# Performance work log

Hardware: AMD Instinct MI355X
Metric: run time of the kernel (lower is better)

The kernel has to match this reference:

```python
import jax, jax.numpy as jnp
import numpy as np

B, S, NX, H = 8, 1024, 1024, 16
HD = NX // H  # head dim = 64
MASKED_BIAS = -10000.0


def setup_inputs() -> dict:
    key = jax.random.key(0)
    ks = jax.random.split(key, 6)
    return {
        "x": jax.random.normal(ks[0], (B, S, NX), dtype=jnp.float32),
        "query": jax.random.normal(ks[1], (B, S, NX), dtype=jnp.float32),
        "c_attn_w": jax.random.normal(ks[2], (NX, 3 * NX), dtype=jnp.float32) * 0.02,
        "c_attn_b": jnp.zeros((3 * NX,), dtype=jnp.float32),
        "c_proj_w": jax.random.normal(ks[3], (NX, NX), dtype=jnp.float32) * 0.02,
        "c_proj_b": jnp.zeros((NX,), dtype=jnp.float32),
    }


def _split_heads(t):
    # [B, S, NX] -> [B, H, S, HD]
    b, s, _ = t.shape
    return t.reshape(b, s, H, HD).transpose(0, 2, 1, 3)


def reference(x, query, c_attn_w, c_attn_b, c_proj_w, c_proj_b):
    # Conv1D: y = x @ W + b
    kv = x @ c_attn_w + c_attn_b          # [B,S,3NX]; use key/value slices
    qy = query @ c_attn_w + c_attn_b      # [B,S,3NX]; use query slice
    q = _split_heads(qy[..., :NX])                     # [B,H,S,HD]
    k = _split_heads(kv[..., NX:2 * NX])               # [B,H,S,HD]
    v = _split_heads(kv[..., 2 * NX:])                 # [B,H,S,HD]

    w = jnp.einsum("bhqd,bhkd->bhqk", q, k) / jnp.sqrt(jnp.float32(HD))
    causal = jnp.tril(jnp.ones((S, S), dtype=bool))[None, None]
    w = jnp.where(causal, w, jnp.float32(MASKED_BIAS))
    w = jax.nn.softmax(w, axis=-1)
    a = jnp.einsum("bhqk,bhkd->bhqd", w, v)            # [B,H,S,HD]
    a = a.transpose(0, 2, 1, 3).reshape(B, S, NX)      # merge heads
    return a @ c_proj_w + c_proj_b
```

## Files before the change

kernel.cpp:

```cpp
#include <hip/hip_runtime.h>
#include <cstdint>
#include <cstddef>

#define Bb   8
#define Ss   1024
#define NXx  1024
#define Hh   16
#define HDd  64
#define Mm   (Bb*Ss)

typedef __bf16 bf16x8 __attribute__((ext_vector_type(8)));
typedef float  f32x4  __attribute__((ext_vector_type(4)));

__device__ __forceinline__ unsigned short f2bf(float f) {
    union { float f; unsigned int u; } v; v.f = f;
    return (unsigned short)((v.u + 0x8000u) >> 16);
}
__device__ __forceinline__ unsigned int f2bf_hi(float f) {
    union { float f; unsigned int u; } v; v.f = f;
    return (v.u + 0x8000u) & 0xffff0000u;
}

__device__ __forceinline__ void load_lds16(const unsigned short* g, unsigned short* lds_base) {
    __builtin_amdgcn_global_load_lds(
        (const __attribute__((address_space(1))) void*)g,
        (__attribute__((address_space(3))) void*)lds_base, 16, 0, 0);
}

__global__ __launch_bounds__(256) void prep(
    const float* __restrict__ x, const float* __restrict__ query,
    const float* __restrict__ caw, const float* __restrict__ cpw,
    unsigned short* __restrict__ xb, unsigned short* __restrict__ qb,
    unsigned short* __restrict__ Wt, unsigned short* __restrict__ Pt)
{
    __shared__ float tile[32][33];
    const int bid = blockIdx.x;
    const int tid = threadIdx.x;

    if (bid < 16384) {
        const float* in = (bid < 8192) ? x : query;
        unsigned short* out = (bid < 8192) ? xb : qb;
        const int i = ((bid & 8191) * 256 + tid) * 4;
        const float4 v = *(const float4*)(in + i);
        unsigned long long p = (unsigned long long)f2bf(v.x)
            | ((unsigned long long)f2bf(v.y) << 16)
            | ((unsigned long long)f2bf(v.z) << 32)
            | ((unsigned long long)f2bf(v.w) << 48);
        *(unsigned long long*)(out + i) = p;
        return;
    }

    const float* in;
    unsigned short* out;
    int C, t;
    if (bid < 16384 + 3072) { in = caw; out = Wt; C = 3072; t = bid - 16384; }
    else                    { in = cpw; out = Pt; C = 1024; t = bid - 19456; }
    const int ntx = C >> 5;
    const int c0 = (t % ntx) * 32, r0 = (t / ntx) * 32;
    const int tx = tid & 31, ty = tid >> 5;
    for (int i = ty; i < 32; i += 8)
        tile[i][tx] = in[(size_t)(r0 + i) * C + c0 + tx];
    __syncthreads();
    for (int i = ty; i < 32; i += 8)
        out[(size_t)(c0 + i) * 1024 + r0 + tx] = f2bf(tile[tx][i]);
}

__global__ __launch_bounds__(256) void gemm128(
    const unsigned short* __restrict__ Ax,
    const unsigned short* __restrict__ Aq,
    const unsigned short* __restrict__ Bt,
    const float* __restrict__ bias,
    int K, int mode,
    unsigned short* __restrict__ out_q,
    unsigned short* __restrict__ out_k,
    unsigned short* __restrict__ out_v,
    float* __restrict__ out_f)
{
    __shared__ unsigned short smem[16384];
    unsigned short (*As)[64] = (unsigned short (*)[64])(smem);
    unsigned short (*Bs)[64] = (unsigned short (*)[64])(smem + 8192);

    const int tid  = threadIdx.x;
    const int w    = tid >> 6;
    const int lane = tid & 63;

    const int nx   = (mode == 0) ? 24 : 8;
    const int nxh  = nx >> 1;
    const int n    = blockIdx.x;
    const int xcd  = n & 7;
    const int sgrp = n >> 3;
    const int m0   = ((xcd >> 1) * 16 + sgrp / nxh) * 128;
    const int n0   = ((xcd & 1) * nxh + sgrp % nxh) * 128;
    const int region = n0 >> 10;
    const unsigned short* A = (mode == 0 && region == 0) ? Aq : Ax;

    const int wm   = (w >> 1) * 64;
    const int wn   = (w & 1) * 64;
    const int lrow = lane & 15;
    const int quad = lane >> 4;

    f32x4 acc[4][4] = {};

    const int rr   = lane >> 3;
    const int scol = (((lane & 7) ^ (lane >> 3)) << 3);
    const unsigned short* Ag = A  + (size_t)(m0 + w * 32 + rr) * K + scol;
    const unsigned short* Bg = Bt + (size_t)(n0 + w * 32 + rr) * K + scol;
    unsigned short* ldsA = smem + (w * 32) * 64;
    unsigned short* ldsB = smem + 8192 + (w * 32) * 64;

    const int swz = lrow & 7;

    for (int k0 = 0; k0 < K; k0 += 64) {
        __syncthreads();
#pragma unroll
        for (int c = 0; c < 4; ++c) {
            load_lds16(Ag + (size_t)(c * 8) * K + k0, ldsA + c * 512);
            load_lds16(Bg + (size_t)(c * 8) * K + k0, ldsB + c * 512);
        }
        __syncthreads();
#pragma unroll
        for (int kk = 0; kk < 2; ++kk) {
            bf16x8 af[4], bfr[4];
            const int pc = (((kk * 4 + quad) ^ swz) << 3);
#pragma unroll
            for (int i = 0; i < 4; ++i) {
                af[i]  = *(const bf16x8*)&As[wm + i * 16 + lrow][pc];
                bfr[i] = *(const bf16x8*)&Bs[wn + i * 16 + lrow][pc];
            }
#pragma unroll
            for (int i = 0; i < 4; ++i)
#pragma unroll
                for (int j = 0; j < 4; ++j)
                    acc[i][j] = __builtin_amdgcn_mfma_f32_16x16x32_bf16(af[i], bfr[j], acc[i][j], 0, 0, 0);
        }
    }

    __syncthreads();

    if (mode == 1) {
#pragma unroll
        for (int i = 0; i < 4; ++i)
#pragma unroll
            for (int j = 0; j < 4; ++j) {
                const int ncol = n0 + wn + j * 16 + lrow;
                const float bv = bias[ncol];
#pragma unroll
                for (int r = 0; r < 4; ++r) {
                    const int mrow = m0 + wm + i * 16 + quad * 4 + r;
                    out_f[(size_t)mrow * NXx + ncol] = acc[i][j][r] + bv;
                }
            }
        return;
    }

    unsigned short* ep = smem + w * 2048;

    if (region != 2) {
        unsigned short* outp = (region == 0) ? out_q : out_k;
#pragma unroll
        for (int j = 0; j < 4; ++j) {
            const float bv = bias[n0 + wn + j * 16 + lrow];
#pragma unroll
            for (int i = 0; i < 4; ++i)
#pragma unroll
                for (int r = 0; r < 4; ++r)
                    ep[(i * 16 + quad * 4 + r) * 24 + lrow] = f2bf(acc[i][j][r] + bv);
#pragma unroll
            for (int t = 0; t < 2; ++t) {
                const int c    = t * 64 + lane;
                const int row  = c >> 1, ch = (c & 1) * 8;
                const int mrow = m0 + wm + row;
                const int cc   = (n0 + wn + j * 16 + ch) & (NXx - 1);
                const int hh   = cc >> 6, dd = cc & 63;
                const int bh   = (mrow >> 10) * Hh + hh;
                const int ss   = mrow & (Ss - 1);
                *(uint4*)&outp[((size_t)bh * Ss + ss) * HDd + dd] =
                    *(const uint4*)&ep[row * 24 + ch];
            }
        }
    } else {
#pragma unroll
        for (int j = 0; j < 4; ++j) {
            const float bv = bias[n0 + wn + j * 16 + lrow];
#pragma unroll
            for (int i = 0; i < 4; ++i)
#pragma unroll
                for (int r = 0; r < 4; ++r)
                    ep[lrow * 72 + i * 16 + quad * 4 + r] = f2bf(acc[i][j][r] + bv);
#pragma unroll
            for (int t = 0; t < 2; ++t) {
                const int c    = t * 64 + lane;
                const int col  = c >> 3, rc = (c & 7) * 8;
                const int cc   = (n0 + wn + j * 16 + col) & (NXx - 1);
                const int hh   = cc >> 6, dd = cc & 63;
                const int mrow = m0 + wm + rc;
                const int bh   = (mrow >> 10) * Hh + hh;
                const int ss   = mrow & (Ss - 1);
                *(uint4*)&out_v[((size_t)bh * HDd + dd) * Ss + ss] =
                    *(const uint4*)&ep[col * 72 + rc];
            }
        }
    }
}

__global__ __launch_bounds__(512, 2) void gemm256(
    const unsigned short* __restrict__ Ax,
    const unsigned short* __restrict__ Aq,
    const unsigned short* __restrict__ Bt,
    const float* __restrict__ bias,
    unsigned short* __restrict__ out_q,
    unsigned short* __restrict__ out_k,
    unsigned short* __restrict__ out_v)
{
    __shared__ unsigned short lds[65536];

    const int tid  = threadIdx.x;
    const int w    = tid >> 6;
    const int lane = tid & 63;
    const int wm   = w >> 2;
    const int wn   = w & 3;
    const int lrow = lane & 15;
    const int quad = lane >> 4;
    const int swz  = lrow & 7;
    const int ca   = (quad ^ swz) << 3;
    const int cb   = ((4 + quad) ^ swz) << 3;

    const int n    = blockIdx.x;
    const int xcd  = n & 7;
    const int sg   = n >> 3;
    const int mi   = (xcd >> 1) * 8 + (sg & 7);
    const int ni   = (xcd & 1) * 6 + (sg >> 3);
    const int m0   = mi << 8;
    const int n0   = ni << 8;
    const int region = n0 >> 10;
    const unsigned short* A = (region == 0) ? Aq : Ax;

    const int srow = lane >> 3;
    const int chnk = (((lane & 7) ^ srow) << 3);
    const unsigned short* pA0 = A  + (size_t)(m0 +       w * 8 + srow) * 1024 + chnk;
    const unsigned short* pA1 = A  + (size_t)(m0 +  64 + w * 8 + srow) * 1024 + chnk;
    const unsigned short* pA2 = A  + (size_t)(m0 + 128 + w * 8 + srow) * 1024 + chnk;
    const unsigned short* pA3 = A  + (size_t)(m0 + 192 + w * 8 + srow) * 1024 + chnk;
    const unsigned short* pB0 = Bt + (size_t)(n0 +       w * 8 + srow) * 1024 + chnk;
    const unsigned short* pB1 = Bt + (size_t)(n0 +  64 + w * 8 + srow) * 1024 + chnk;
    const unsigned short* pB2 = Bt + (size_t)(n0 + 128 + w * 8 + srow) * 1024 + chnk;
    const unsigned short* pB3 = Bt + (size_t)(n0 + 192 + w * 8 + srow) * 1024 + chnk;
    const int wl = w * 512;

    f32x4 acc[8][4] = {};

    load_lds16(pA0, lds + 0 * 4096 + wl);
    load_lds16(pA2, lds + 2 * 4096 + wl);
    load_lds16(pB0, lds + 16384 + 0 * 4096 + wl);
    load_lds16(pB1, lds + 16384 + 1 * 4096 + wl);
    load_lds16(pB2, lds + 16384 + 2 * 4096 + wl);
    load_lds16(pB3, lds + 16384 + 3 * 4096 + wl);
    load_lds16(pA1, lds + 1 * 4096 + wl);
    load_lds16(pA3, lds + 3 * 4096 + wl);
    pA0 += 64; pA1 += 64; pA2 += 64; pA3 += 64;
    pB0 += 64; pB1 += 64; pB2 += 64; pB3 += 64;

    asm volatile("s_waitcnt vmcnt(2)" ::: "memory");
    __builtin_amdgcn_s_barrier();
    asm volatile("" ::: "memory");

#pragma unroll 1
    for (int t = 0; t < 16; ++t) {
        const int as = (t & 1) << 15;
        const int us = ((t & 1) ^ 1) << 15;
        const bool st = (t < 15);
        const int rbA = as + (wm * 128 + lrow) * 64;
        const int rbB = as + 16384 + (wn * 64 + lrow) * 64;

        bf16x8 a0f[4], a1f[4], b0q[4], b1q[4];

#pragma unroll
        for (int i = 0; i < 4; ++i) a0f[i] = *(const bf16x8*)&lds[rbA + i * 1024 + ca];
#pragma unroll
        for (int j = 0; j < 4; ++j) b0q[j] = *(const bf16x8*)&lds[rbB + j * 1024 + ca];
        if (st) {
            load_lds16(pA0, lds + us + 0 * 4096 + wl);
            load_lds16(pA2, lds + us + 2 * 4096 + wl);
            load_lds16(pB0, lds + us + 16384 + 0 * 4096 + wl);
        }
        __builtin_amdgcn_s_barrier();
        asm volatile("s_waitcnt lgkmcnt(0)" ::: "memory");
        __builtin_amdgcn_s_setprio(1);
#pragma unroll
        for (int i = 0; i < 4; ++i)
#pragma unroll
            for (int j = 0; j < 4; ++j)
                acc[i][j] = __builtin_amdgcn_mfma_f32_16x16x32_bf16(a0f[i], b0q[j], acc[i][j], 0, 0, 0);
        __builtin_amdgcn_s_setprio(0);
        asm volatile("" ::: "memory");
        __builtin_amdgcn_s_barrier();
        asm volatile("" ::: "memory");

#pragma unroll
        for (int i = 0; i < 4; ++i) a1f[i] = *(const bf16x8*)&lds[rbA + i * 1024 + cb];
#pragma unroll
        for (int j = 0; j < 4; ++j) b1q[j] = *(const bf16x8*)&lds[rbB + j * 1024 + cb];
        if (st) {
            load_lds16(pB1, lds + us + 16384 + 1 * 4096 + wl);
            load_lds16(pB2, lds + us + 16384 + 2 * 4096 + wl);
            load_lds16(pB3, lds + us + 16384 + 3 * 4096 + wl);
        }
        __builtin_amdgcn_s_barrier();
        asm volatile("s_waitcnt lgkmcnt(0)" ::: "memory");
        __builtin_amdgcn_s_setprio(1);
#pragma unroll
        for (int i = 0; i < 4; ++i)
#pragma unroll
            for (int j = 0; j < 4; ++j)
                acc[i][j] = __builtin_amdgcn_mfma_f32_16x16x32_bf16(a1f[i], b1q[j], acc[i][j], 0, 0, 0);
        __builtin_amdgcn_s_setprio(0);
        if (st) asm volatile("s_waitcnt vmcnt(6)" ::: "memory");
        else    asm volatile("s_waitcnt vmcnt(0)" ::: "memory");
        asm volatile("" ::: "memory");
        __builtin_amdgcn_s_barrier();
        asm volatile("" ::: "memory");

#pragma unroll
        for (int i = 0; i < 4; ++i) a0f[i] = *(const bf16x8*)&lds[rbA + 4096 + i * 1024 + ca];
        __builtin_amdgcn_s_barrier();
        asm volatile("s_waitcnt lgkmcnt(0)" ::: "memory");
        __builtin_amdgcn_s_setprio(1);
#pragma unroll
        for (int i = 0; i < 4; ++i)
#pragma unroll
            for (int j = 0; j < 4; ++j)
                acc[4 + i][j] = __builtin_amdgcn_mfma_f32_16x16x32_bf16(a0f[i], b0q[j], acc[4 + i][j], 0, 0, 0);
        __builtin_amdgcn_s_setprio(0);
        asm volatile("" ::: "memory");
        __builtin_amdgcn_s_barrier();
        asm volatile("" ::: "memory");

#pragma unroll
        for (int i = 0; i < 4; ++i) a1f[i] = *(const bf16x8*)&lds[rbA + 4096 + i * 1024 + cb];
        if (st) {
            load_lds16(pA1, lds + us + 1 * 4096 + wl);
            load_lds16(pA3, lds + us + 3 * 4096 + wl);
            pA0 += 64; pA1 += 64; pA2 += 64; pA3 += 64;
            pB0 += 64; pB1 += 64; pB2 += 64; pB3 += 64;
        }
        __builtin_amdgcn_s_barrier();
        asm volatile("s_waitcnt lgkmcnt(0)" ::: "memory");
        __builtin_amdgcn_s_setprio(1);
#pragma unroll
        for (int i = 0; i < 4; ++i)
#pragma unroll
            for (int j = 0; j < 4; ++j)
                acc[4 + i][j] = __builtin_amdgcn_mfma_f32_16x16x32_bf16(a1f[i], b1q[j], acc[4 + i][j], 0, 0, 0);
        __builtin_amdgcn_s_setprio(0);
        if (st) asm volatile("s_waitcnt vmcnt(2)" ::: "memory");
        asm volatile("" ::: "memory");
        __builtin_amdgcn_s_barrier();
        asm volatile("" ::: "memory");
    }

    __syncthreads();

    unsigned short* ep = lds + w * 8192;

    if (region != 2) {
        unsigned short* outp = (region == 0) ? out_q : out_k;
#pragma unroll
        for (int j = 0; j < 4; ++j) {
            const float bv = bias[n0 + wn * 64 + j * 16 + lrow];
#pragma unroll
            for (int i = 0; i < 8; ++i)
#pragma unroll
                for (int r = 0; r < 4; ++r)
                    ep[(i * 16 + quad * 4 + r) * 24 + lrow] = f2bf(acc[i][j][r] + bv);
#pragma unroll
            for (int tt = 0; tt < 4; ++tt) {
                const int c    = tt * 64 + lane;
                const int row  = c >> 1, ch = (c & 1) * 8;
                const int mrow = m0 + wm * 128 + row;
                const int cc   = (n0 + wn * 64 + j * 16 + ch) & (NXx - 1);
                const int hh   = cc >> 6, dd = cc & 63;
                const int bh   = (mrow >> 10) * Hh + hh;
                const int ss   = mrow & (Ss - 1);
                *(uint4*)&outp[((size_t)bh * Ss + ss) * HDd + dd] =
                    *(const uint4*)&ep[row * 24 + ch];
            }
        }
    } else {
#pragma unroll
        for (int j = 0; j < 4; ++j) {
            const float bv = bias[n0 + wn * 64 + j * 16 + lrow];
#pragma unroll
            for (int i = 0; i < 8; ++i)
#pragma unroll
                for (int r = 0; r < 4; ++r)
                    ep[lrow * 136 + i * 16 + quad * 4 + r] = f2bf(acc[i][j][r] + bv);
#pragma unroll
            for (int tt = 0; tt < 4; ++tt) {
                const int c    = tt * 64 + lane;
                const int col  = c >> 4, rc = (c & 15) * 8;
                const int cc   = (n0 + wn * 64 + j * 16 + col) & (NXx - 1);
                const int hh   = cc >> 6, dd = cc & 63;
                const int mrow = m0 + wm * 128 + rc;
                const int bh   = (mrow >> 10) * Hh + hh;
                const int ss   = mrow & (Ss - 1);
                *(uint4*)&out_v[((size_t)bh * HDd + dd) * Ss + ss] =
                    *(const uint4*)&ep[col * 136 + rc];
            }
        }
    }
}

__global__ __launch_bounds__(256) void flash_attn(
    const unsigned short* __restrict__ Qh,
    const unsigned short* __restrict__ Kh,
    const unsigned short* __restrict__ Vt,
    unsigned short* __restrict__ about)
{
    __shared__ unsigned short Ks[64][64];
    __shared__ unsigned short Vs[64][64];
    __shared__ unsigned short Pl[4][32][72];

    const int tid  = threadIdx.x;
    const int w    = tid >> 6;
    const int lane = tid & 63;
    const int bh   = blockIdx.x & 127;
    const int pr   = blockIdx.x >> 7;
    const int b    = bh >> 4, h = bh & 15;
    const int lrow = lane & 15;
    const int quad = lane >> 4;

    const unsigned short* Qb = Qh + (size_t)bh * Ss * HDd;
    const unsigned short* Kb = Kh + (size_t)bh * Ss * HDd;
    const unsigned short* Vb = Vt + (size_t)bh * HDd * Ss;

    const int sr = lane >> 3;
    const int lc = (((lane & 7) ^ (lane >> 3)) << 3);
    unsigned short* ldsK0 = &Ks[w * 16][0];
    unsigned short* ldsK1 = &Ks[w * 16 + 8][0];
    unsigned short* ldsV0 = &Vs[w * 16][0];
    unsigned short* ldsV1 = &Vs[w * 16 + 8][0];

    const int swz = lrow & 7;
    const int ca = ((quad ^ swz) << 3);
    const int cb = (((4 + quad) ^ swz) << 3);

    for (int half = 0; half < 2; ++half) {
        const int qt = half ? (7 - pr) : pr;
        const int qw = qt * 128 + w * 32;

        bf16x8 aq[2][2];
#pragma unroll
        for (int g = 0; g < 2; ++g)
#pragma unroll
            for (int c = 0; c < 2; ++c)
                aq[g][c] = *(const bf16x8*)(Qb + (size_t)(qw + g * 16 + lrow) * HDd + c * 32 + quad * 8);

        f32x4 O[2][4] = {};
        float lsum[2] = { 0.f, 0.f };

        const int nkt = 2 * qt + 2;
        for (int kt = 0; kt < nkt; ++kt) {
            const int k0 = kt * 64;

            __syncthreads();
            load_lds16(Kb + (size_t)(k0 + w * 16 + sr) * HDd + lc,     ldsK0);
            load_lds16(Kb + (size_t)(k0 + w * 16 + sr + 8) * HDd + lc, ldsK1);
            load_lds16(Vb + (size_t)(w * 16 + sr) * Ss + k0 + lc,      ldsV0);
            load_lds16(Vb + (size_t)(w * 16 + sr + 8) * Ss + k0 + lc,  ldsV1);
            __syncthreads();

            if (k0 > qw + 31) continue;

            f32x4 st[2][4] = {};
#pragma unroll
            for (int j = 0; j < 4; ++j) {
                const bf16x8 kf0 = *(const bf16x8*)&Ks[j * 16 + lrow][ca];
                const bf16x8 kf1 = *(const bf16x8*)&Ks[j * 16 + lrow][cb];
                st[0][j] = __builtin_amdgcn_mfma_f32_16x16x32_bf16(kf0, aq[0][0], st[0][j], 0, 0, 0);
                st[0][j] = __builtin_amdgcn_mfma_f32_16x16x32_bf16(kf1, aq[0][1], st[0][j], 0, 0, 0);
                st[1][j] = __builtin_amdgcn_mfma_f32_16x16x32_bf16(kf0, aq[1][0], st[1][j], 0, 0, 0);
                st[1][j] = __builtin_amdgcn_mfma_f32_16x16x32_bf16(kf1, aq[1][1], st[1][j], 0, 0, 0);
            }

            const bool needMask = (k0 + 63 > qw);
#pragma unroll
            for (int g = 0; g < 2; ++g) {
                const int qg = qw + g * 16 + lrow;
#pragma unroll
                for (int j = 0; j < 4; ++j) {
                    const int kbase = k0 + j * 16 + quad * 4;
                    float e0 = __expf(st[g][j][0] * 0.125f);
                    float e1 = __expf(st[g][j][1] * 0.125f);
                    float e2 = __expf(st[g][j][2] * 0.125f);
                    float e3 = __expf(st[g][j][3] * 0.125f);
                    if (needMask) {
                        if (kbase     > qg) e0 = 0.f;
                        if (kbase + 1 > qg) e1 = 0.f;
                        if (kbase + 2 > qg) e2 = 0.f;
                        if (kbase + 3 > qg) e3 = 0.f;
                    }
                    lsum[g] += (e0 + e1) + (e2 + e3);
                    uint2 pk;
                    pk.x = (unsigned)f2bf(e0) | f2bf_hi(e1);
                    pk.y = (unsigned)f2bf(e2) | f2bf_hi(e3);
                    *(uint2*)&Pl[w][g * 16 + lrow][j * 16 + quad * 4] = pk;
                }
            }

            bf16x8 ap[2][2];
#pragma unroll
            for (int g = 0; g < 2; ++g)
#pragma unroll
                for (int c = 0; c < 2; ++c)
                    ap[g][c] = *(const bf16x8*)&Pl[w][g * 16 + lrow][c * 32 + quad * 8];
#pragma unroll
            for (int f = 0; f < 4; ++f) {
                const bf16x8 vf0 = *(const bf16x8*)&Vs[f * 16 + lrow][ca];
                const bf16x8 vf1 = *(const bf16x8*)&Vs[f * 16 + lrow][cb];
                O[0][f] = __builtin_amdgcn_mfma_f32_16x16x32_bf16(ap[0][0], vf0, O[0][f], 0, 0, 0);
                O[0][f] = __builtin_amdgcn_mfma_f32_16x16x32_bf16(ap[0][1], vf1, O[0][f], 0, 0, 0);
                O[1][f] = __builtin_amdgcn_mfma_f32_16x16x32_bf16(ap[1][0], vf0, O[1][f], 0, 0, 0);
                O[1][f] = __builtin_amdgcn_mfma_f32_16x16x32_bf16(ap[1][1], vf1, O[1][f], 0, 0, 0);
            }
        }

#pragma unroll
        for (int g = 0; g < 2; ++g) {
            float l = lsum[g];
            l += __shfl_xor(l, 16);
            l += __shfl_xor(l, 32);
            const float inv = 1.0f / l;
#pragma unroll
            for (int r = 0; r < 4; ++r) {
                const float invr = __shfl(inv, quad * 4 + r);
                const int q = qw + g * 16 + quad * 4 + r;
                const size_t base = ((size_t)b * Ss + q) * NXx + h * HDd;
#pragma unroll
                for (int f = 0; f < 4; ++f)
                    about[base + f * 16 + lrow] = f2bf(O[g][f][r] * invr);
            }
        }
    }
}

extern "C" void kernel_launch(void* const* d_in, const int* in_sizes, int n_in,
                              void* d_out, int out_size, void* d_ws, size_t ws_size,
                              hipStream_t stream) {
    const float* x        = (const float*)d_in[0];
    const float* query    = (const float*)d_in[1];
    const float* c_attn_w = (const float*)d_in[2];
    const float* c_attn_b = (const float*)d_in[3];
    const float* c_proj_w = (const float*)d_in[4];
    const float* c_proj_b = (const float*)d_in[5];
    float* out = (float*)d_out;

    const size_t nTok = (size_t)Mm * NXx;
    char* ws = (char*)d_ws;
    unsigned short* xb    = (unsigned short*)ws;                 ws += nTok * 2;
    unsigned short* qb    = (unsigned short*)ws;                 ws += nTok * 2;
    unsigned short* Wt    = (unsigned short*)ws;                 ws += (size_t)3 * NXx * NXx * 2;
    unsigned short* Pt    = (unsigned short*)ws;                 ws += (size_t)NXx * NXx * 2;
    unsigned short* Qh    = (unsigned short*)ws;                 ws += nTok * 2;
    unsigned short* Kh    = (unsigned short*)ws;                 ws += nTok * 2;
    unsigned short* Vt    = (unsigned short*)ws;                 ws += nTok * 2;
    unsigned short* about = (unsigned short*)ws;                 ws += nTok * 2;
    if ((size_t)(ws - (char*)d_ws) > ws_size) return;

    prep<<<20480, 256, 0, stream>>>(x, query, c_attn_w, c_proj_w, xb, qb, Wt, Pt);

    gemm256<<<384, 512, 0, stream>>>(xb, qb, Wt, c_attn_b, Qh, Kh, Vt);

    flash_attn<<<512, 256, 0, stream>>>(Qh, Kh, Vt, about);

    gemm128<<<dim3(8 * 64), 256, 0, stream>>>(about, nullptr, Pt, c_proj_b, NXx, 1,
                                              nullptr, nullptr, nullptr, out);
}
```

Baseline: 264.1 us.

## Shrink QKV GEMM tile to 256x128 and merge K-half phases

The QKV projection GEMM moves from 256x256 to 256x128 output tiles. This doubles the grid to 768 blocks, shrinks LDS to 96KB and halves the per-warp accumulators. Each sub-step now loads both K-halves of its fragments at once, which removes half of the barrier/MFMA phases per iteration. The aim is better occupancy and load balance across CUs, at the cost of lower arithmetic intensity and more global traffic for the A operand.

After: 255.9 us. -3.1%, faster.

```diff
diff --git a/kernel.cpp b/kernel.cpp
--- a/kernel.cpp
+++ b/kernel.cpp
@@ -212,13 +212,13 @@
     unsigned short* __restrict__ out_k,
     unsigned short* __restrict__ out_v)
 {
-    __shared__ unsigned short lds[65536];
+    __shared__ unsigned short lds[49152];
 
     const int tid  = threadIdx.x;
     const int w    = tid >> 6;
     const int lane = tid & 63;
-    const int wm   = w >> 2;
-    const int wn   = w & 3;
+    const int wm   = (w >> 2) * 128;
+    const int wn   = (w & 3) * 32;
     const int lrow = lane & 15;
     const int quad = lane >> 4;
     const int swz  = lrow & 7;
@@ -229,9 +229,9 @@
     const int xcd  = n & 7;
     const int sg   = n >> 3;
     const int mi   = (xcd >> 1) * 8 + (sg & 7);
-    const int ni   = (xcd & 1) * 6 + (sg >> 3);
+    const int ni   = (xcd & 1) * 12 + (sg >> 3);
     const int m0   = mi << 8;
-    const int n0   = ni << 8;
+    const int n0   = ni << 7;
     const int region = n0 >> 10;
     const unsigned short* A = (region == 0) ? Aq : Ax;
 
@@ -243,22 +243,18 @@
     const unsigned short* pA3 = A  + (size_t)(m0 + 192 + w * 8 + srow) * 1024 + chnk;
     const unsigned short* pB0 = Bt + (size_t)(n0 +       w * 8 + srow) * 1024 + chnk;
     const unsigned short* pB1 = Bt + (size_t)(n0 +  64 + w * 8 + srow) * 1024 + chnk;
-    const unsigned short* pB2 = Bt + (size_t)(n0 + 128 + w * 8 + srow) * 1024 + chnk;
-    const unsigned short* pB3 = Bt + (size_t)(n0 + 192 + w * 8 + srow) * 1024 + chnk;
     const int wl = w * 512;
 
-    f32x4 acc[8][4] = {};
+    f32x4 acc[8][2] = {};
 
     load_lds16(pA0, lds + 0 * 4096 + wl);
     load_lds16(pA2, lds + 2 * 4096 + wl);
-    load_lds16(pB0, lds + 16384 + 0 * 4096 + wl);
-    load_lds16(pB1, lds + 16384 + 1 * 4096 + wl);
-    load_lds16(pB2, lds + 16384 + 2 * 4096 + wl);
-    load_lds16(pB3, lds + 16384 + 3 * 4096 + wl);
+    load_lds16(pB0, lds + 32768 + 0 * 4096 + wl);
+    load_lds16(pB1, lds + 32768 + 1 * 4096 + wl);
     load_lds16(pA1, lds + 1 * 4096 + wl);
     load_lds16(pA3, lds + 3 * 4096 + wl);
     pA0 += 64; pA1 += 64; pA2 += 64; pA3 += 64;
-    pB0 += 64; pB1 += 64; pB2 += 64; pB3 += 64;
+    pB0 += 64; pB1 += 64;
 
     asm volatile("s_waitcnt vmcnt(2)" ::: "memory");
     __builtin_amdgcn_s_barrier();
@@ -266,22 +262,31 @@
 
 #pragma unroll 1
     for (int t = 0; t < 16; ++t) {
-        const int as = (t & 1) << 15;
-        const int us = ((t & 1) ^ 1) << 15;
+        const int ab = (t & 1) * 16384;
+        const int bb = 32768 + (t & 1) * 8192;
+        const int ua = ((t & 1) ^ 1) * 16384;
+        const int ub = 32768 + ((t & 1) ^ 1) * 8192;
         const bool st = (t < 15);
-        const int rbA = as + (wm * 128 + lrow) * 64;
-        const int rbB = as + 16384 + (wn * 64 + lrow) * 64;
-
-        bf16x8 a0f[4], a1f[4], b0q[4], b1q[4];
-
-#pragma unroll
-        for (int i = 0; i < 4; ++i) a0f[i] = *(const bf16x8*)&lds[rbA + i * 1024 + ca];
-#pragma unroll
-        for (int j = 0; j < 4; ++j) b0q[j] = *(const bf16x8*)&lds[rbB + j * 1024 + ca];
+        const int rbA = ab + (wm + lrow) * 64;
+        const int rbB = bb + (wn + lrow) * 64;
+
+        bf16x8 a0f[4], a1f[4], b0q[2], b1q[2];
+
+#pragma unroll
+        for (int i = 0; i < 4; ++i) {
+            a0f[i] = *(const bf16x8*)&lds[rbA + i * 1024 + ca];
+            a1f[i] = *(const bf16x8*)&lds[rbA + i * 1024 + cb];
+        }
+#pragma unroll
+        for (int j = 0; j < 2; ++j) {
+            b0q[j] = *(const bf16x8*)&lds[rbB + j * 1024 + ca];
+            b1q[j] = *(const bf16x8*)&lds[rbB + j * 1024 + cb];
+        }
         if (st) {
-            load_lds16(pA0, lds + us + 0 * 4096 + wl);
-            load_lds16(pA2, lds + us + 2 * 4096 + wl);
-            load_lds16(pB0, lds + us + 16384 + 0 * 4096 + wl);
+            load_lds16(pA0, lds + ua + 0 * 4096 + wl);
+            load_lds16(pA2, lds + ua + 2 * 4096 + wl);
+            load_lds16(pB0, lds + ub + 0 * 4096 + wl);
+            load_lds16(pB1, lds + ub + 1 * 4096 + wl);
         }
         __builtin_amdgcn_s_barrier();
         asm volatile("s_waitcnt lgkmcnt(0)" ::: "memory");
@@ -289,67 +294,43 @@
 #pragma unroll
         for (int i = 0; i < 4; ++i)
 #pragma unroll
-            for (int j = 0; j < 4; ++j)
+            for (int j = 0; j < 2; ++j)
                 acc[i][j] = __builtin_amdgcn_mfma_f32_16x16x32_bf16(a0f[i], b0q[j], acc[i][j], 0, 0, 0);
-        __builtin_amdgcn_s_setprio(0);
-        asm volatile("" ::: "memory");
-        __builtin_amdgcn_s_barrier();
-        asm volatile("" ::: "memory");
-
-#pragma unroll
-        for (int i = 0; i < 4; ++i) a1f[i] = *(const bf16x8*)&lds[rbA + i * 1024 + cb];
-#pragma unroll
-        for (int j = 0; j < 4; ++j) b1q[j] = *(const bf16x8*)&lds[rbB + j * 1024 + cb];
-        if (st) {
-            load_lds16(pB1, lds + us + 16384 + 1 * 4096 + wl);
-            load_lds16(pB2, lds + us + 16384 + 2 * 4096 + wl);
-            load_lds16(pB3, lds + us + 16384 + 3 * 4096 + wl);
-        }
-        __builtin_amdgcn_s_barrier();
-        asm volatile("s_waitcnt lgkmcnt(0)" ::: "memory");
-        __builtin_amdgcn_s_setprio(1);
 #pragma unroll
         for (int i = 0; i < 4; ++i)
 #pragma unroll
-            for (int j = 0; j < 4; ++j)
+            for (int j = 0; j < 2; ++j)
                 acc[i][j] = __builtin_amdgcn_mfma_f32_16x16x32_bf16(a1f[i], b1q[j], acc[i][j], 0, 0, 0);
         __builtin_amdgcn_s_setprio(0);
-        if (st) asm volatile("s_waitcnt vmcnt(6)" ::: "memory");
+        if (st) asm volatile("s_waitcnt vmcnt(4)" ::: "memory");
         else    asm volatile("s_waitcnt vmcnt(0)" ::: "memory");
         asm volatile("" ::: "memory");
         __builtin_amdgcn_s_barrier();
         asm volatile("" ::: "memory");
 
 #pragma unroll
-        for (int i = 0; i < 4; ++i) a0f[i] = *(const bf16x8*)&lds[rbA + 4096 + i * 1024 + ca];
+        for (int i = 0; i < 4; ++i) {
+            a0f[i] = *(const bf16x8*)&lds[rbA + 4096 + i * 1024 + ca];
+            a1f[i] = *(const bf16x8*)&lds[rbA + 4096 + i * 1024 + cb];
+        }
+        if (st) {
+            load_lds16(pA1, lds + ua + 1 * 4096 + wl);
+            load_lds16(pA3, lds + ua + 3 * 4096 + wl);
+            pA0 += 64; pA1 += 64; pA2 += 64; pA3 += 64;
+            pB0 += 64; pB1 += 64;
+        }
         __builtin_amdgcn_s_barrier();
         asm volatile("s_waitcnt lgkmcnt(0)" ::: "memory");
         __builtin_amdgcn_s_setprio(1);
 #pragma unroll
         for (int i = 0; i < 4; ++i)
 #pragma unroll
-            for (int j = 0; j < 4; ++j)
+            for (int j = 0; j < 2; ++j)
                 acc[4 + i][j] = __builtin_amdgcn_mfma_f32_16x16x32_bf16(a0f[i], b0q[j], acc[4 + i][j], 0, 0, 0);
-        __builtin_amdgcn_s_setprio(0);
-        asm volatile("" ::: "memory");
-        __builtin_amdgcn_s_barrier();
-        asm volatile("" ::: "memory");
-
-#pragma unroll
-        for (int i = 0; i < 4; ++i) a1f[i] = *(const bf16x8*)&lds[rbA + 4096 + i * 1024 + cb];
-        if (st) {
-            load_lds16(pA1, lds + us + 1 * 4096 + wl);
-            load_lds16(pA3, lds + us + 3 * 4096 + wl);
-            pA0 += 64; pA1 += 64; pA2 += 64; pA3 += 64;
-            pB0 += 64; pB1 += 64; pB2 += 64; pB3 += 64;
-        }
-        __builtin_amdgcn_s_barrier();
-        asm volatile("s_waitcnt lgkmcnt(0)" ::: "memory");
-        __builtin_amdgcn_s_setprio(1);
 #pragma unroll
         for (int i = 0; i < 4; ++i)
 #pragma unroll
-            for (int j = 0; j < 4; ++j)
+            for (int j = 0; j < 2; ++j)
                 acc[4 + i][j] = __builtin_amdgcn_mfma_f32_16x16x32_bf16(a1f[i], b1q[j], acc[4 + i][j], 0, 0, 0);
         __builtin_amdgcn_s_setprio(0);
         if (st) asm volatile("s_waitcnt vmcnt(2)" ::: "memory");
@@ -360,13 +341,13 @@
 
     __syncthreads();
 
-    unsigned short* ep = lds + w * 8192;
+    unsigned short* ep = lds + w * 6144;
 
     if (region != 2) {
         unsigned short* outp = (region == 0) ? out_q : out_k;
 #pragma unroll
-        for (int j = 0; j < 4; ++j) {
-            const float bv = bias[n0 + wn * 64 + j * 16 + lrow];
+        for (int j = 0; j < 2; ++j) {
+            const float bv = bias[n0 + wn + j * 16 + lrow];
 #pragma unroll
             for (int i = 0; i < 8; ++i)
 #pragma unroll
@@ -376,8 +357,8 @@
             for (int tt = 0; tt < 4; ++tt) {
                 const int c    = tt * 64 + lane;
                 const int row  = c >> 1, ch = (c & 1) * 8;
-                const int mrow = m0 + wm * 128 + row;
-                const int cc   = (n0 + wn * 64 + j * 16 + ch) & (NXx - 1);
+                const int mrow = m0 + wm + row;
+                const int cc   = (n0 + wn + j * 16 + ch) & (NXx - 1);
                 const int hh   = cc >> 6, dd = cc & 63;
                 const int bh   = (mrow >> 10) * Hh + hh;
                 const int ss   = mrow & (Ss - 1);
@@ -387,8 +368,8 @@
         }
     } else {
 #pragma unroll
-        for (int j = 0; j < 4; ++j) {
-            const float bv = bias[n0 + wn * 64 + j * 16 + lrow];
+        for (int j = 0; j < 2; ++j) {
+            const float bv = bias[n0 + wn + j * 16 + lrow];
 #pragma unroll
             for (int i = 0; i < 8; ++i)
 #pragma unroll
@@ -398,9 +379,9 @@
             for (int tt = 0; tt < 4; ++tt) {
                 const int c    = tt * 64 + lane;
                 const int col  = c >> 4, rc = (c & 15) * 8;
-                const int cc   = (n0 + wn * 64 + j * 16 + col) & (NXx - 1);
+                const int cc   = (n0 + wn + j * 16 + col) & (NXx - 1);
                 const int hh   = cc >> 6, dd = cc & 63;
-                const int mrow = m0 + wm * 128 + rc;
+                const int mrow = m0 + wm + rc;
                 const int bh   = (mrow >> 10) * Hh + hh;
                 const int ss   = mrow & (Ss - 1);
                 *(uint4*)&out_v[((size_t)bh * HDd + dd) * Ss + ss] =
@@ -568,7 +549,7 @@
 
     prep<<<20480, 256, 0, stream>>>(x, query, c_attn_w, c_proj_w, xb, qb, Wt, Pt);
 
-    gemm256<<<384, 512, 0, stream>>>(xb, qb, Wt, c_attn_b, Qh, Kh, Vt);
+    gemm256<<<768, 512, 0, stream>>>(xb, qb, Wt, c_attn_b, Qh, Kh, Vt);
 
     flash_attn<<<512, 256, 0, stream>>>(Qh, Kh, Vt, about);
 
```
